# Optimization experiments

Measured on AMD Instinct MI355X. Metric: run time of the kernel, lower is better.

Reference implementation:

```python
import jax, jax.numpy as jnp
import numpy as np

WINDOWS = [2, 4, 6]
THR = 0.5


def conv1x1(x, w, b):
    # x: [N,C,H,W], w: [O,C], b: [O]
    return jnp.einsum('nchw,oc->nohw', x, w) + b[None, :, None, None]


def cpool(x):
    # channel max + mean -> [N,2,H,W]
    return jnp.stack([x.max(axis=1), x.mean(axis=1)], axis=1)


def mask_fusion(orin, feature, w1, b1, w2, b2):
    sim = jax.nn.sigmoid(jnp.sum(conv1x1(cpool(orin), w1, b1) * conv1x1(cpool(feature), w2, b2), axis=1, keepdims=True))
    mask = (sim > THR).astype(orin.dtype)
    return mask * feature + (1.0 - mask) * orin


def unfold(x, kh, kw, sh, sw, w):
    # torch F.unfold equivalent -> [N, C*kh*kw, w*w] (channel-major like torch)
    rows = jnp.arange(w)[:, None] * sh + jnp.arange(kh)[None, :]  # [w,kh]
    cols = jnp.arange(w)[:, None] * sw + jnp.arange(kw)[None, :]  # [w,kw]
    p = x[:, :, rows[:, :, None, None], cols[None, None, :, :]]  # [N,C,w,kh,w,kw]
    p = p.transpose(0, 1, 3, 5, 2, 4)  # [N,C,kh,kw,w,w]
    N, C = x.shape[:2]
    return p.reshape(N, C * kh * kw, w * w)


def fold(cols_, H, W, kh, kw, sh, sw, w):
    # torch F.fold equivalent (col2im with overlap-add)
    N, CK, P = cols_.shape
    C = CK // (kh * kw)
    p = cols_.reshape(N, C, kh, kw, w, w).transpose(0, 1, 4, 2, 5, 3).reshape(N, C, w * kh, w * kw)
    r = (jnp.arange(w)[:, None] * sh + jnp.arange(kh)[None, :]).reshape(-1)
    c = (jnp.arange(w)[:, None] * sw + jnp.arange(kw)[None, :]).reshape(-1)
    return jnp.zeros((N, C, H, W), cols_.dtype).at[:, :, r[:, None], c[None, :]].add(p)


def psa(u, wq, wk, wv):
    # u: [N,C,P,L]; scaled dot-product self-attention over L within each patch
    t = u.transpose(0, 2, 3, 1)  # [N,P,L,C]
    q, k, v = t @ wq, t @ wk, t @ wv
    s = jnp.einsum('nplc,npmc->nplm', q, k) / jnp.sqrt(jnp.asarray(t.shape[-1], t.dtype))
    o = jnp.einsum('nplm,npmc->nplc', jax.nn.softmax(s, axis=-1), v)
    return o.transpose(0, 3, 1, 2)


def setup_inputs():
    key = jax.random.key(0)
    ks = jax.random.split(key, 20)
    N, C, H, W = 4, 64, 72, 72
    E = len(WINDOWS) * C
    nrm = lambda k, shape, s: jax.random.normal(k, shape, jnp.float32) * s
    return {
        'x': nrm(ks[0], (N, C, H, W), 1.0),
        'exp_w': nrm(ks[1], (E, C), C ** -0.5), 'exp_b': jnp.zeros((E,), jnp.float32),
        'res_w': nrm(ks[2], (C, E), E ** -0.5), 'res_b': jnp.zeros((C,), jnp.float32),
        'fus_w': nrm(ks[3], (C, C), C ** -0.5), 'fus_b': jnp.zeros((C,), jnp.float32),
        'wq': nrm(ks[4], (C, C), C ** -0.5),
        'wk': nrm(ks[5], (C, C), C ** -0.5),
        'wv': nrm(ks[6], (C, C), C ** -0.5),
        'mf1a_w': nrm(ks[7], (2, 2), 0.7), 'mf1a_b': jnp.zeros((2,), jnp.float32),
        'mf1b_w': nrm(ks[8], (2, 2), 0.7), 'mf1b_b': jnp.zeros((2,), jnp.float32),
        'mf2a_w': nrm(ks[9], (2, 2), 0.7), 'mf2a_b': jnp.zeros((2,), jnp.float32),
        'mf2b_w': nrm(ks[10], (2, 2), 0.7), 'mf2b_b': jnp.zeros((2,), jnp.float32),
    }


def reference(x, exp_w, exp_b, res_w, res_b, fus_w, fus_b, wq, wk, wv,
              mf1a_w, mf1a_b, mf1b_w, mf1b_b, mf2a_w, mf2a_b, mf2b_w, mf2b_b):
    N, C, H, W = x.shape
    expx = conv1x1(x, exp_w, exp_b)  # [N, 3C, H, W]
    parts = jnp.split(expx, len(WINDOWS), axis=1)
    outs = []
    for i, w in enumerate(WINDOWS):
        sh, sw = H // w, W // w
        kh, kw = sh + H % w, sw + W % w
        u = unfold(parts[i], kh, kw, sh, sw, w)       # [N, C*kh*kw, w*w]
        u = u.reshape(N, C, w * w, kh * kw)           # raw reinterpret, as in torch .view
        a = psa(u, wq, wk, wv).reshape(N, C * kh * kw, w * w)
        cnt = fold(jnp.ones_like(a), H, W, kh, kw, sh, sw, w)
        outs.append(fold(a, H, W, kh, kw, sh, sw, w) / cnt)
    out = mask_fusion(jnp.concatenate(outs, axis=1), expx, mf1a_w, mf1a_b, mf1b_w, mf1b_b)
    out = conv1x1(out, res_w, res_b)
    out = mask_fusion(out, x, mf2a_w, mf2a_b, mf2b_w, mf2b_b)
    return conv1x1(out, fus_w, fus_b)
```

## Files before the change

kernel.cpp:

```cpp
#include <hip/hip_runtime.h>

constexpr int CN = 4;
constexpr int CC = 64;
constexpr int CH = 72, CW = 72;
constexpr int HW = CH * CW;
constexpr int NPOS = CN * HW;
constexpr long TOKF = 3L * NPOS * 64;
constexpr long HPAD = 4096;

typedef _Float16 h4 __attribute__((ext_vector_type(4)));
typedef _Float16 h8 __attribute__((ext_vector_type(8)));
typedef float f4 __attribute__((ext_vector_type(4)));

__device__ __forceinline__ int fidx(int row, int g, int off) {
  return (row << 6) + ((g ^ (row & 7)) << 3) + off;
}
__device__ __forceinline__ int f192(int row, int g) {
  return row * 192 + (((g & 24) | ((g ^ row) & 7)) << 3);
}

template <int WW, int SS>
__device__ __forceinline__ void expand_body(const float* __restrict__ x,
                                            const float* __restrict__ w64,
                                            const float* __restrict__ b64,
                                            float* __restrict__ out, int pg,
                                            int og0) {
  int n = pg / HW;
  int pos = pg - n * HW;
  int h = pos / CW, wcol = pos % CW;

  float xv[64];
  const float* xp = x + (long)n * CC * HW + pos;
#pragma unroll
  for (int c = 0; c < 64; ++c) xv[c] = xp[c * HW];

  int wr = h / SS, kx = h % SS, wcq = wcol / SS, ky = wcol % SS;
  int j = kx * (SS * WW * WW) + ky * (WW * WW) + wr * WW + wcq;
  float* op = out + ((long)n * HW + j) * 64;

#pragma unroll
  for (int og = og0; og < og0 + 4; ++og) {
    float t0[4];
#pragma unroll
    for (int i = 0; i < 4; ++i) {
      int o = og * 4 + i;
      float acc = b64[o];
      const float* wp = w64 + o * 64;
#pragma unroll
      for (int cg = 0; cg < 16; ++cg) {
        float4 w4 = *(const float4*)(wp + 4 * cg);
        acc = fmaf(xv[4 * cg + 0], w4.x, acc);
        acc = fmaf(xv[4 * cg + 1], w4.y, acc);
        acc = fmaf(xv[4 * cg + 2], w4.z, acc);
        acc = fmaf(xv[4 * cg + 3], w4.w, acc);
      }
      t0[i] = acc;
    }
    *(float4*)(op + og * 4) = make_float4(t0[0], t0[1], t0[2], t0[3]);
  }
}

__global__ __launch_bounds__(256) void k_prep(
    const float* __restrict__ x, const float* __restrict__ exp_w,
    const float* __restrict__ exp_b, const float* __restrict__ wq,
    const float* __restrict__ wk, const float* __restrict__ wv,
    const float* __restrict__ res_w, const float* __restrict__ fus_w,
    float* __restrict__ ex, _Float16* __restrict__ wTh,
    _Float16* __restrict__ wTl, _Float16* __restrict__ rwh,
    _Float16* __restrict__ rwl, _Float16* __restrict__ fwh,
    _Float16* __restrict__ fwl) {
  int b = blockIdx.x;
  if (b >= 972) {
    int i = (b - 972) * 256 + threadIdx.x;
    float v;
    _Float16 *dh, *dl;
    int off;
    if (i < 12288) {
      int m = i >> 12;
      int r = i & 4095;
      int cp = r >> 6, c = r & 63;
      const float* src = (m == 0) ? wq : ((m == 1) ? wk : wv);
      v = src[c * 64 + cp];
      dh = wTh; dl = wTl; off = i;
    } else if (i < 24576) {
      off = i - 12288;
      v = res_w[off];
      dh = rwh; dl = rwl;
    } else {
      off = i - 24576;
      v = fus_w[off];
      dh = fwh; dl = fwl;
    }
    _Float16 h = (_Float16)v;
    dh[off] = h;
    dl[off] = (_Float16)(v - (float)h);
    return;
  }
  int wi = b / 324;
  int b2 = b - wi * 324;
  int og0 = (b2 / 81) * 4;
  int pg = (b2 % 81) * 256 + threadIdx.x;
  if (wi == 0)
    expand_body<2, 36>(x, exp_w, exp_b, ex, pg, og0);
  else if (wi == 1)
    expand_body<4, 18>(x, exp_w + 4096, exp_b + 64, ex + (long)NPOS * 64, pg,
                       og0);
  else
    expand_body<6, 12>(x, exp_w + 8192, exp_b + 128, ex + 2L * NPOS * 64, pg,
                       og0);
}

__global__ __launch_bounds__(256) void k_qkv(
    const float* __restrict__ ex, const _Float16* __restrict__ wTh,
    const _Float16* __restrict__ wTl, _Float16* __restrict__ qh,
    _Float16* __restrict__ ql, _Float16* __restrict__ kh,
    _Float16* __restrict__ kl, _Float16* __restrict__ vth,
    _Float16* __restrict__ vtl) {
  __shared__ __align__(16) _Float16 Wh[12288], Wl[12288];
  __shared__ __align__(16) float Cb[4096];
  _Float16* Eh = (_Float16*)Cb;
  _Float16* El = (_Float16*)Cb + 4096;

  const int tid = threadIdx.x;
  const long tok0 = (long)blockIdx.x * 64;
  const int lane = tid & 63, w = tid >> 6;
  const int lw = lane & 15, lg = lane >> 4;

  {
    int srow = tid >> 2, sfq = tid & 3;
#pragma unroll
    for (int p = 0; p < 4; ++p) {
      int c0 = (4 * p + sfq) * 4;
      float4 v = *(const float4*)(ex + (tok0 + srow) * 64 + c0);
      h4 hh = {(_Float16)v.x, (_Float16)v.y, (_Float16)v.z, (_Float16)v.w};
      h4 ll = {(_Float16)(v.x - (float)hh[0]), (_Float16)(v.y - (float)hh[1]),
               (_Float16)(v.z - (float)hh[2]), (_Float16)(v.w - (float)hh[3])};
      *(h4*)&Eh[fidx(srow, c0 >> 3, c0 & 7)] = hh;
      *(h4*)&El[fidx(srow, c0 >> 3, c0 & 7)] = ll;
    }
  }
#pragma unroll
  for (int it = 0; it < 6; ++it) {
    int idx = it * 256 + tid;
    int row = idx >> 3, gr = idx & 7;
    *(h8*)&Wh[fidx(row, gr, 0)] = *(const h8*)(wTh + idx * 8);
    *(h8*)&Wl[fidx(row, gr, 0)] = *(const h8*)(wTl + idx * 8);
  }
  __syncthreads();

  h8 eh[2], el[2];
#pragma unroll
  for (int s = 0; s < 2; ++s) {
    eh[s] = *(const h8*)&Eh[fidx(w * 16 + lw, s * 4 + lg, 0)];
    el[s] = *(const h8*)&El[fidx(w * 16 + lw, s * 4 + lg, 0)];
  }
  __syncthreads();

  const float SC = 0.125f * 1.4426950408889634f;
#pragma unroll 1
  for (int p = 0; p < 3; ++p) {
#pragma unroll
    for (int ot = 0; ot < 4; ++ot) {
      f4 acc = (f4){0.f, 0.f, 0.f, 0.f};
#pragma unroll
      for (int s = 0; s < 2; ++s) {
        h8 bh = *(const h8*)&Wh[fidx(p * 64 + ot * 16 + lw, s * 4 + lg, 0)];
        h8 bl = *(const h8*)&Wl[fidx(p * 64 + ot * 16 + lw, s * 4 + lg, 0)];
        acc = __builtin_amdgcn_mfma_f32_16x16x32_f16(eh[s], bh, acc, 0, 0, 0);
        acc = __builtin_amdgcn_mfma_f32_16x16x32_f16(el[s], bh, acc, 0, 0, 0);
        acc = __builtin_amdgcn_mfma_f32_16x16x32_f16(eh[s], bl, acc, 0, 0, 0);
      }
#pragma unroll
      for (int r = 0; r < 4; ++r) {
        int row = w * 16 + 4 * lg + r;
        int col = ot * 16 + lw;
        Cb[(row << 6) + ((((col >> 2) ^ (row & 15))) << 2) + (col & 3)] =
            acc[r];
      }
    }
    __syncthreads();

    if (p < 2) {
      int tokl = tid >> 2, off = (tid & 3) * 16;
      float vals[16];
#pragma unroll
      for (int j = 0; j < 4; ++j) {
        int slot = (off >> 2) + j;
        f4 v = *(const f4*)&Cb[(tokl << 6) + (((slot ^ (tokl & 15))) << 2)];
        vals[4 * j + 0] = v[0]; vals[4 * j + 1] = v[1];
        vals[4 * j + 2] = v[2]; vals[4 * j + 3] = v[3];
      }
      float sc = (p == 0) ? SC : 1.0f;
      _Float16* dh = (p == 0 ? qh : kh) + (tok0 + tokl) * 64 + off;
      _Float16* dl = (p == 0 ? ql : kl) + (tok0 + tokl) * 64 + off;
      h8 hh0, hh1, ll0, ll1;
#pragma unroll
      for (int j = 0; j < 8; ++j) {
        float x0 = vals[j] * sc;
        _Float16 h = (_Float16)x0;
        hh0[j] = h;
        ll0[j] = (_Float16)(x0 - (float)h);
        float x1 = vals[8 + j] * sc;
        _Float16 h1 = (_Float16)x1;
        hh1[j] = h1;
        ll1[j] = (_Float16)(x1 - (float)h1);
      }
      *(h8*)dh = hh0; *(h8*)(dh + 8) = hh1;
      *(h8*)dl = ll0; *(h8*)(dl + 8) = ll1;
    } else {
      int ch0 = (tid & 15) * 4, tokl0 = (tid >> 4) * 4;
      float tv[4][4];
#pragma unroll
      for (int r = 0; r < 4; ++r) {
        int row = tokl0 + r;
        int slot = (ch0 >> 2) ^ (row & 15);
        f4 v = *(const f4*)&Cb[(row << 6) + (slot << 2)];
        tv[r][0] = v[0]; tv[r][1] = v[1]; tv[r][2] = v[2]; tv[r][3] = v[3];
      }
      long tokg = tok0 + tokl0;
      int wi = (int)(tokg / NPOS);
      long tl = tokg - (long)wi * NPOS;
      int L = (wi == 0) ? 1296 : ((wi == 1) ? 324 : 144);
      int g = (int)(tl / L);
      int key0 = (int)(tl - (long)g * L);
      long base = (long)wi * NPOS * 64 + (long)g * 64 * L + key0;
#pragma unroll
      for (int i = 0; i < 4; ++i) {
        h4 hh, ll;
#pragma unroll
        for (int r = 0; r < 4; ++r) {
          _Float16 h = (_Float16)tv[r][i];
          hh[r] = h;
          ll[r] = (_Float16)(tv[r][i] - (float)h);
        }
        *(h4*)&vth[base + (long)(ch0 + i) * L] = hh;
        *(h4*)&vtl[base + (long)(ch0 + i) * L] = ll;
      }
    }
    __syncthreads();
  }
}

__global__ __launch_bounds__(256) void k_attn(
    const _Float16* __restrict__ qg, const _Float16* __restrict__ qgl,
    const _Float16* __restrict__ kg, const _Float16* __restrict__ kgl,
    const _Float16* __restrict__ vg, const _Float16* __restrict__ vgl,
    float* __restrict__ og_) {
  __shared__ __align__(16) _Float16 Kh[4096], Kl[4096];
  __shared__ __align__(16) _Float16 Vh[4096], Vl[4096];
  __shared__ __align__(16) _Float16 Ph[4096], Pl[4096];

  const int tid = threadIdx.x;
  int b = blockIdx.x;
  int L, g, qt, NCH;
  long tokbase, vbase;
  if (b < 336) {
    L = 1296; NCH = 21; g = b & 15; qt = b >> 4;
    tokbase = (long)g * 1296;
    vbase = (long)g * 1296 * 64;
  } else if (b < 720) {
    int t = b - 336;
    L = 324; NCH = 6; g = t & 63; qt = t >> 6;
    tokbase = (long)NPOS + (long)g * 324;
    vbase = (long)NPOS * 64 + (long)g * 324 * 64;
  } else {
    int t = b - 720;
    L = 144; NCH = 3; g = t % 144; qt = t / 144;
    tokbase = 2L * NPOS + (long)g * 144;
    vbase = 2L * NPOS * 64 + (long)g * 144 * 64;
  }

  const int lane = tid & 63, w = tid >> 6;
  const int lw = lane & 15, lg = lane >> 4;
  const int w16 = w * 16;

  h8 qfh[2], qfl[2];
  {
    long qb = (tokbase + (long)qt * 64 + w16 + lw) * 64;
#pragma unroll
    for (int s = 0; s < 2; ++s) {
      qfh[s] = *(const h8*)(qg + qb + (s * 4 + lg) * 8);
      qfl[s] = *(const h8*)(qgl + qb + (s * 4 + lg) * 8);
    }
  }

  float m_s = -1e30f, l_s = 0.f;
  f4 oa[4];
#pragma unroll
  for (int i = 0; i < 4; ++i) oa[i] = (f4){0.f, 0.f, 0.f, 0.f};

  const int krow = tid >> 3, kgr = tid & 7;
  const long ksA = (tokbase + krow) * 64 + kgr * 8;
  const long vsA = vbase + (long)krow * L + kgr * 8;
  const long v32 = (long)32 * L;

  h8 rk0, rk1, rl0, rl1, rv0, rv1, rw0, rw1;
  auto loadKV = [&](int chn) {
    long ko = ksA + ((long)chn << 12);
    long vo = vsA + chn * 64;
    rk0 = *(const h8*)(kg + ko);
    rl0 = *(const h8*)(kgl + ko);
    rv0 = *(const h8*)(vg + vo);
    rw0 = *(const h8*)(vgl + vo);
    rk1 = *(const h8*)(kg + ko + 2048);
    rl1 = *(const h8*)(kgl + ko + 2048);
    rv1 = *(const h8*)(vg + vo + v32);
    rw1 = *(const h8*)(vgl + vo + v32);
  };
  loadKV(0);

  for (int ch = 0; ch < NCH; ++ch) {
    __syncthreads();
    {
      *(h8*)&Kh[fidx(krow, kgr, 0)] = rk0;
      *(h8*)&Kl[fidx(krow, kgr, 0)] = rl0;
      *(h8*)&Vh[fidx(krow, kgr, 0)] = rv0;
      *(h8*)&Vl[fidx(krow, kgr, 0)] = rw0;
      *(h8*)&Kh[fidx(32 + krow, kgr, 0)] = rk1;
      *(h8*)&Kl[fidx(32 + krow, kgr, 0)] = rl1;
      *(h8*)&Vh[fidx(32 + krow, kgr, 0)] = rv1;
      *(h8*)&Vl[fidx(32 + krow, kgr, 0)] = rw1;
    }
    __syncthreads();
    if (ch + 1 < NCH) loadKV(ch + 1);

    f4 sa[4];
#pragma unroll
    for (int kt = 0; kt < 4; ++kt) sa[kt] = (f4){0.f, 0.f, 0.f, 0.f};
#pragma unroll
    for (int slab = 0; slab < 2; ++slab) {
      h8 qbh = qfh[slab];
      h8 qbl = qfl[slab];
#pragma unroll
      for (int kt = 0; kt < 4; ++kt) {
        h8 ah = *(const h8*)&Kh[fidx(kt * 16 + lw, slab * 4 + lg, 0)];
        h8 al = *(const h8*)&Kl[fidx(kt * 16 + lw, slab * 4 + lg, 0)];
        sa[kt] = __builtin_amdgcn_mfma_f32_16x16x32_f16(ah, qbh, sa[kt], 0, 0, 0);
        sa[kt] = __builtin_amdgcn_mfma_f32_16x16x32_f16(al, qbh, sa[kt], 0, 0, 0);
        sa[kt] = __builtin_amdgcn_mfma_f32_16x16x32_f16(ah, qbl, sa[kt], 0, 0, 0);
      }
    }

    float pr[4][4];
    float pmax = -1e30f;
#pragma unroll
    for (int kt = 0; kt < 4; ++kt)
#pragma unroll
      for (int r = 0; r < 4; ++r) {
        int kidx = ch * 64 + kt * 16 + 4 * lg + r;
        float s = (kidx < L) ? sa[kt][r] : -1e30f;
        pr[kt][r] = s;
        pmax = fmaxf(pmax, s);
      }
    pmax = fmaxf(pmax, __shfl_xor(pmax, 16));
    pmax = fmaxf(pmax, __shfl_xor(pmax, 32));
    if (!__all(pmax <= m_s + 8.0f)) {
      float mn = fmaxf(m_s, pmax);
      float fs = exp2f(m_s - mn);
      m_s = mn;
      float fsb[4];
#pragma unroll
      for (int r = 0; r < 4; ++r) fsb[r] = __shfl(fs, 4 * lg + r);
#pragma unroll
      for (int ct = 0; ct < 4; ++ct)
#pragma unroll
        for (int r = 0; r < 4; ++r) oa[ct][r] *= fsb[r];
      l_s *= fs;
    }
    float rs = 0.f;
#pragma unroll
    for (int kt = 0; kt < 4; ++kt)
#pragma unroll
      for (int r = 0; r < 4; ++r) {
        float e = exp2f(pr[kt][r] - m_s);
        pr[kt][r] = e;
        rs += e;
      }
    rs += __shfl_xor(rs, 16);
    rs += __shfl_xor(rs, 32);
    l_s += rs;

#pragma unroll
    for (int kt = 0; kt < 4; ++kt) {
      h4 hh = {(_Float16)pr[kt][0], (_Float16)pr[kt][1], (_Float16)pr[kt][2],
               (_Float16)pr[kt][3]};
      h4 ll = {(_Float16)(pr[kt][0] - (float)hh[0]),
               (_Float16)(pr[kt][1] - (float)hh[1]),
               (_Float16)(pr[kt][2] - (float)hh[2]),
               (_Float16)(pr[kt][3] - (float)hh[3])};
      int key0 = kt * 16 + 4 * lg;
      int kgr2 = key0 >> 3, ko = key0 & 7;
      *(h4*)&Ph[fidx(w16 + lw, kgr2, ko)] = hh;
      *(h4*)&Pl[fidx(w16 + lw, kgr2, ko)] = ll;
    }

#pragma unroll
    for (int slab = 0; slab < 2; ++slab) {
      h8 pah = *(const h8*)&Ph[fidx(w16 + lw, slab * 4 + lg, 0)];
      h8 pal = *(const h8*)&Pl[fidx(w16 + lw, slab * 4 + lg, 0)];
#pragma unroll
      for (int ct = 0; ct < 4; ++ct) {
        h8 vbh = *(const h8*)&Vh[fidx(ct * 16 + lw, slab * 4 + lg, 0)];
        h8 vbl = *(const h8*)&Vl[fidx(ct * 16 + lw, slab * 4 + lg, 0)];
        oa[ct] = __builtin_amdgcn_mfma_f32_16x16x32_f16(pah, vbh, oa[ct], 0, 0, 0);
        oa[ct] = __builtin_amdgcn_mfma_f32_16x16x32_f16(pal, vbh, oa[ct], 0, 0, 0);
        oa[ct] = __builtin_amdgcn_mfma_f32_16x16x32_f16(pah, vbl, oa[ct], 0, 0, 0);
      }
    }
  }

  float linv[4];
#pragma unroll
  for (int r = 0; r < 4; ++r) linv[r] = 1.0f / __shfl(l_s, 4 * lg + r);
#pragma unroll
  for (int r = 0; r < 4; ++r) {
    int qi = qt * 64 + w16 + 4 * lg + r;
    if (qi < L) {
      float* op = og_ + (tokbase + qi) * 64 + lw;
#pragma unroll
      for (int ct = 0; ct < 4; ++ct) op[ct * 16] = oa[ct][r] * linv[r];
    }
  }
}

__global__ __launch_bounds__(256) void k_fuse3(
    const float* __restrict__ x, const float* __restrict__ ex,
    const float* __restrict__ att, const float* __restrict__ m1aw,
    const float* __restrict__ m1ab, const float* __restrict__ m1bw,
    const float* __restrict__ m1bb, const _Float16* __restrict__ rwh,
    const _Float16* __restrict__ rwl, const float* __restrict__ res_b,
    const _Float16* __restrict__ fwh, const _Float16* __restrict__ fwl,
    const float* __restrict__ fus_b, const float* __restrict__ m2aw,
    const float* __restrict__ m2ab, const float* __restrict__ m2bw,
    const float* __restrict__ m2bb, float* __restrict__ out) {
  __shared__ __align__(16) _Float16 F1hS[12288];
  __shared__ __align__(16) _Float16 F1lS[12288];
  float* Cb = (float*)F1hS;
  _Float16* o2h = F1lS;
  _Float16* o2l = F1lS + 4096;

  const int tid = threadIdx.x;
  const int posb = blockIdx.x * 64;
  const int n = posb / HW, posn = posb % HW;
  const int lane = tid & 63, w = tid >> 6;
  const int lw = lane & 15, lg = lane >> 4;
  const int w16 = w * 16;

  {
    float w1a0 = m1aw[0], w1a1 = m1aw[1], w1a2 = m1aw[2], w1a3 = m1aw[3];
    float b1a0 = m1ab[0], b1a1 = m1ab[1];
    float w1b0 = m1bw[0], w1b1 = m1bw[1], w1b2 = m1bw[2], w1b3 = m1bw[3];
    float b1b0 = m1bb[0], b1b1 = m1bb[1];
#pragma unroll 2
    for (int pp = 0; pp < 16; ++pp) {
      int pl = w * 16 + pp;
      int pos = posn + pl;
      int h = pos / CW, wcol = pos % CW;
      auto tok = [&](int S, int W) -> int {
        int wr = h / S, kx = h % S, wcq = wcol / S, ky = wcol % S;
        return kx * (S * W * W) + ky * (W * W) + wr * W + wcq;
      };
      int j0 = tok(36, 2), j1 = tok(18, 4), j2 = tok(12, 6);
      long t0 = ((long)n * HW + j0) * 64 + lane;
      long t1 = ((long)NPOS + (long)n * HW + j1) * 64 + lane;
      long t2 = (2L * NPOS + (long)n * HW + j2) * 64 + lane;
      float av0 = att[t0], av1 = att[t1], av2 = att[t2];
      float ev0 = ex[t0], ev1 = ex[t1], ev2 = ex[t2];
      float mxa = fmaxf(fmaxf(av0, av1), av2), sma = av0 + av1 + av2;
      float mxe = fmaxf(fmaxf(ev0, ev1), ev2), sme = ev0 + ev1 + ev2;
#pragma unroll
      for (int d = 1; d < 64; d <<= 1) {
        mxa = fmaxf(mxa, __shfl_xor(mxa, d));
        sma += __shfl_xor(sma, d);
        mxe = fmaxf(mxe, __shfl_xor(mxe, d));
        sme += __shfl_xor(sme, d);
      }
      float mna = sma * (1.f / 192.f), mne = sme * (1.f / 192.f);
      float ca0 = fmaf(w1a0, mxa, fmaf(w1a1, mna, b1a0));
      float ca1 = fmaf(w1a2, mxa, fmaf(w1a3, mna, b1a1));
      float cb0 = fmaf(w1b0, mxe, fmaf(w1b1, mne, b1b0));
      float cb1 = fmaf(w1b2, mxe, fmaf(w1b3, mne, b1b1));
      bool mk = (ca0 * cb0 + ca1 * cb1) > 0.f;
      float v0 = mk ? ev0 : av0;
      float v1 = mk ? ev1 : av1;
      float v2 = mk ? ev2 : av2;
      _Float16 h0 = (_Float16)v0, h1 = (_Float16)v1, h2 = (_Float16)v2;
      int c0 = lane, c1 = lane + 64, c2 = lane + 128;
      F1hS[f192(pl, c0 >> 3) + (c0 & 7)] = h0;
      F1lS[f192(pl, c0 >> 3) + (c0 & 7)] = (_Float16)(v0 - (float)h0);
      F1hS[f192(pl, c1 >> 3) + (c1 & 7)] = h1;
      F1lS[f192(pl, c1 >> 3) + (c1 & 7)] = (_Float16)(v1 - (float)h1);
      F1hS[f192(pl, c2 >> 3) + (c2 & 7)] = h2;
      F1lS[f192(pl, c2 >> 3) + (c2 & 7)] = (_Float16)(v2 - (float)h2);
    }
  }
  __syncthreads();

  h8 ah[6], al[6];
#pragma unroll
  for (int s = 0; s < 6; ++s) {
    ah[s] = *(const h8*)&F1hS[f192(w16 + lw, s * 4 + lg)];
    al[s] = *(const h8*)&F1lS[f192(w16 + lw, s * 4 + lg)];
  }

  f4 acc[4];
#pragma unroll
  for (int ot = 0; ot < 4; ++ot) {
    float bb = res_b[ot * 16 + lw];
    acc[ot] = (f4){bb, bb, bb, bb};
#pragma unroll
    for (int s = 0; s < 6; ++s) {
      int wo = (ot * 16 + lw) * 192 + (s * 4 + lg) * 8;
      h8 bh = *(const h8*)(rwh + wo);
      h8 bl = *(const h8*)(rwl + wo);
      acc[ot] = __builtin_amdgcn_mfma_f32_16x16x32_f16(ah[s], bh, acc[ot], 0, 0, 0);
      acc[ot] = __builtin_amdgcn_mfma_f32_16x16x32_f16(al[s], bh, acc[ot], 0, 0, 0);
      acc[ot] = __builtin_amdgcn_mfma_f32_16x16x32_f16(ah[s], bl, acc[ot], 0, 0, 0);
    }
  }
  __syncthreads();

#pragma unroll
  for (int ot = 0; ot < 4; ++ot)
#pragma unroll
    for (int r = 0; r < 4; ++r) {
      int row = w16 + 4 * lg + r, col = ot * 16 + lw;
      Cb[(row << 6) + ((((col >> 2) ^ (row & 15))) << 2) + (col & 3)] =
          acc[ot][r];
    }
  __syncthreads();

  const int pos = tid >> 2, off = (tid & 3) * 16;
  float vals[16];
#pragma unroll
  for (int j = 0; j < 4; ++j) {
    int slot = (off >> 2) + j;
    f4 v = *(const f4*)&Cb[(pos << 6) + (((slot ^ (pos & 15))) << 2)];
    vals[4 * j + 0] = v[0]; vals[4 * j + 1] = v[1];
    vals[4 * j + 2] = v[2]; vals[4 * j + 3] = v[3];
  }
  float amx = vals[0], asum = vals[0];
#pragma unroll
  for (int i = 1; i < 16; ++i) {
    amx = fmaxf(amx, vals[i]);
    asum += vals[i];
  }
  amx = fmaxf(amx, __shfl_xor(amx, 1)); asum += __shfl_xor(asum, 1);
  amx = fmaxf(amx, __shfl_xor(amx, 2)); asum += __shfl_xor(asum, 2);
  float xv[16];
  const float* xp = x + ((long)n * CC + off) * HW + posn + pos;
#pragma unroll
  for (int i = 0; i < 16; ++i) xv[i] = xp[i * HW];
  float xmx = xv[0], xsum = xv[0];
#pragma unroll
  for (int i = 1; i < 16; ++i) {
    xmx = fmaxf(xmx, xv[i]);
    xsum += xv[i];
  }
  xmx = fmaxf(xmx, __shfl_xor(xmx, 1)); xsum += __shfl_xor(xsum, 1);
  xmx = fmaxf(xmx, __shfl_xor(xmx, 2)); xsum += __shfl_xor(xsum, 2);
  float rmn = asum * (1.f / 64.f), xmn = xsum * (1.f / 64.f);
  float ca0 = fmaf(m2aw[0], amx, fmaf(m2aw[1], rmn, m2ab[0]));
  float ca1 = fmaf(m2aw[2], amx, fmaf(m2aw[3], rmn, m2ab[1]));
  float cb0 = fmaf(m2bw[0], xmx, fmaf(m2bw[1], xmn, m2bb[0]));
  float cb1 = fmaf(m2bw[2], xmx, fmaf(m2bw[3], xmn, m2bb[1]));
  bool mk2 = (ca0 * cb0 + ca1 * cb1) > 0.f;

#pragma unroll
  for (int hf = 0; hf < 2; ++hf) {
    h8 hh, ll;
#pragma unroll
    for (int j = 0; j < 8; ++j) {
      float v = mk2 ? xv[hf * 8 + j] : vals[hf * 8 + j];
      _Float16 hx = (_Float16)v;
      hh[j] = hx;
      ll[j] = (_Float16)(v - (float)hx);
    }
    int g = (off >> 3) + hf;
    *(h8*)&o2h[fidx(pos, g, 0)] = hh;
    *(h8*)&o2l[fidx(pos, g, 0)] = ll;
  }
  __syncthreads();

  h8 a2h[2], a2l[2];
#pragma unroll
  for (int s = 0; s < 2; ++s) {
    a2h[s] = *(const h8*)&o2h[fidx(w16 + lw, s * 4 + lg, 0)];
    a2l[s] = *(const h8*)&o2l[fidx(w16 + lw, s * 4 + lg, 0)];
  }
  f4 acc2[4];
#pragma unroll
  for (int ot = 0; ot < 4; ++ot) {
    float bb = fus_b[ot * 16 + lw];
    acc2[ot] = (f4){bb, bb, bb, bb};
#pragma unroll
    for (int s = 0; s < 2; ++s) {
      int wo = (ot * 16 + lw) * 64 + (s * 4 + lg) * 8;
      h8 bh = *(const h8*)(fwh + wo);
      h8 bl = *(const h8*)(fwl + wo);
      acc2[ot] = __builtin_amdgcn_mfma_f32_16x16x32_f16(a2h[s], bh, acc2[ot], 0, 0, 0);
      acc2[ot] = __builtin_amdgcn_mfma_f32_16x16x32_f16(a2l[s], bh, acc2[ot], 0, 0, 0);
      acc2[ot] = __builtin_amdgcn_mfma_f32_16x16x32_f16(a2h[s], bl, acc2[ot], 0, 0, 0);
    }
  }
  __syncthreads();

#pragma unroll
  for (int ot = 0; ot < 4; ++ot)
#pragma unroll
    for (int r = 0; r < 4; ++r) {
      int prow = w16 + 4 * lg + r, col = ot * 16 + lw;
      Cb[(prow << 6) + ((col + prow) & 63)] = acc2[ot][r];
    }
  __syncthreads();
#pragma unroll
  for (int i = 0; i < 16; ++i) {
    float v = Cb[(lane << 6) + ((w16 + i + lane) & 63)];
    out[((long)n * CC + w16 + i) * HW + posn + lane] = v;
  }
}

extern "C" void kernel_launch(void* const* d_in, const int* in_sizes, int n_in,
                              void* d_out, int out_size, void* d_ws,
                              size_t ws_size, hipStream_t stream) {
  (void)in_sizes; (void)n_in; (void)out_size;
  const float* x      = (const float*)d_in[0];
  const float* exp_w  = (const float*)d_in[1];
  const float* exp_b  = (const float*)d_in[2];
  const float* res_w  = (const float*)d_in[3];
  const float* res_b  = (const float*)d_in[4];
  const float* fus_w  = (const float*)d_in[5];
  const float* fus_b  = (const float*)d_in[6];
  const float* wq     = (const float*)d_in[7];
  const float* wk     = (const float*)d_in[8];
  const float* wv     = (const float*)d_in[9];
  const float* m1aw   = (const float*)d_in[10];
  const float* m1ab   = (const float*)d_in[11];
  const float* m1bw   = (const float*)d_in[12];
  const float* m1bb   = (const float*)d_in[13];
  const float* m2aw   = (const float*)d_in[14];
  const float* m2ab   = (const float*)d_in[15];
  const float* m2bw   = (const float*)d_in[16];
  const float* m2bb   = (const float*)d_in[17];

  const long HSZ = TOKF + HPAD;
  const size_t needF =
      2 * (size_t)TOKF + (6 * (size_t)HSZ + 2 * 12288 + 2 * 12288 + 2 * 4096) / 2;
  if (ws_size < needF * sizeof(float)) return;
  float* ws = (float*)d_ws;
  float* ex = ws;
  float* ob = ex + TOKF;
  _Float16* qh  = (_Float16*)(ob + TOKF);
  _Float16* ql  = qh + HSZ;
  _Float16* kh  = ql + HSZ;
  _Float16* kl  = kh + HSZ;
  _Float16* vth = kl + HSZ;
  _Float16* vtl = vth + HSZ;
  _Float16* wTh = vtl + HSZ;
  _Float16* wTl = wTh + 12288;
  _Float16* rwh = wTl + 12288;
  _Float16* rwl = rwh + 12288;
  _Float16* fwh = rwl + 12288;
  _Float16* fwl = fwh + 4096;

  k_prep<<<1084, 256, 0, stream>>>(x, exp_w, exp_b, wq, wk, wv, res_w, fus_w,
                                   ex, wTh, wTl, rwh, rwl, fwh, fwl);
  k_qkv<<<972, 256, 0, stream>>>(ex, wTh, wTl, qh, ql, kh, kl, vth, vtl);
  k_attn<<<1152, 256, 0, stream>>>(qh, ql, kh, kl, vth, vtl, ob);
  k_fuse3<<<324, 256, 0, stream>>>(x, ex, ob, m1aw, m1ab, m1bw, m1bb, rwh,
                                   rwl, res_b, fwh, fwl, fus_b, m2aw, m2ab,
                                   m2bw, m2bb, (float*)d_out);
}
```

Baseline: 139.6 us.

## Load attention K/V MFMA fragments directly from global memory instead of LDS

The attention kernel no longer stages K and V tiles through shared memory with register prefetch and two barriers per chunk. Each wave now reads its MFMA operand fragments for K and V straight from global memory, relying on L1/L2 caching for reuse across the four waves in a block. This removes the LDS writes, the barriers and 32KB of LDS, which may raise occupancy. In exchange every wave issues its own global loads, with no software prefetch to hide their latency.

```diff
diff --git a/kernel.cpp b/kernel.cpp
--- a/kernel.cpp
+++ b/kernel.cpp
@@ -246,8 +246,6 @@
     const _Float16* __restrict__ kg, const _Float16* __restrict__ kgl,
     const _Float16* __restrict__ vg, const _Float16* __restrict__ vgl,
     float* __restrict__ og_) {
-  __shared__ __align__(16) _Float16 Kh[4096], Kl[4096];
-  __shared__ __align__(16) _Float16 Vh[4096], Vl[4096];
   __shared__ __align__(16) _Float16 Ph[4096], Pl[4096];
 
   const int tid = threadIdx.x;
@@ -289,40 +287,13 @@
 #pragma unroll
   for (int i = 0; i < 4; ++i) oa[i] = (f4){0.f, 0.f, 0.f, 0.f};
 
-  const int krow = tid >> 3, kgr = tid & 7;
-  const long ksA = (tokbase + krow) * 64 + kgr * 8;
-  const long vsA = vbase + (long)krow * L + kgr * 8;
-  const long v32 = (long)32 * L;
-
-  h8 rk0, rk1, rl0, rl1, rv0, rv1, rw0, rw1;
-  auto loadKV = [&](int chn) {
-    long ko = ksA + ((long)chn << 12);
-    long vo = vsA + chn * 64;
-    rk0 = *(const h8*)(kg + ko);
-    rl0 = *(const h8*)(kgl + ko);
-    rv0 = *(const h8*)(vg + vo);
-    rw0 = *(const h8*)(vgl + vo);
-    rk1 = *(const h8*)(kg + ko + 2048);
-    rl1 = *(const h8*)(kgl + ko + 2048);
-    rv1 = *(const h8*)(vg + vo + v32);
-    rw1 = *(const h8*)(vgl + vo + v32);
-  };
-  loadKV(0);
+  const long kfb = (tokbase + lw) * 64 + lg * 8;
+  const long vfb = vbase + (long)lw * L + lg * 8;
+  const long vctL = (long)16 * L;
 
   for (int ch = 0; ch < NCH; ++ch) {
-    __syncthreads();
-    {
-      *(h8*)&Kh[fidx(krow, kgr, 0)] = rk0;
-      *(h8*)&Kl[fidx(krow, kgr, 0)] = rl0;
-      *(h8*)&Vh[fidx(krow, kgr, 0)] = rv0;
-      *(h8*)&Vl[fidx(krow, kgr, 0)] = rw0;
-      *(h8*)&Kh[fidx(32 + krow, kgr, 0)] = rk1;
-      *(h8*)&Kl[fidx(32 + krow, kgr, 0)] = rl1;
-      *(h8*)&Vh[fidx(32 + krow, kgr, 0)] = rv1;
-      *(h8*)&Vl[fidx(32 + krow, kgr, 0)] = rw1;
-    }
-    __syncthreads();
-    if (ch + 1 < NCH) loadKV(ch + 1);
+    const long kc = kfb + ((long)ch << 12);
+    const long vc = vfb + ch * 64;
 
     f4 sa[4];
 #pragma unroll
@@ -333,8 +304,9 @@
       h8 qbl = qfl[slab];
 #pragma unroll
       for (int kt = 0; kt < 4; ++kt) {
-        h8 ah = *(const h8*)&Kh[fidx(kt * 16 + lw, slab * 4 + lg, 0)];
-        h8 al = *(const h8*)&Kl[fidx(kt * 16 + lw, slab * 4 + lg, 0)];
+        long ka = kc + kt * 1024 + slab * 32;
+        h8 ah = *(const h8*)(kg + ka);
+        h8 al = *(const h8*)(kgl + ka);
         sa[kt] = __builtin_amdgcn_mfma_f32_16x16x32_f16(ah, qbh, sa[kt], 0, 0, 0);
         sa[kt] = __builtin_amdgcn_mfma_f32_16x16x32_f16(al, qbh, sa[kt], 0, 0, 0);
         sa[kt] = __builtin_amdgcn_mfma_f32_16x16x32_f16(ah, qbl, sa[kt], 0, 0, 0);
@@ -400,8 +372,9 @@
       h8 pal = *(const h8*)&Pl[fidx(w16 + lw, slab * 4 + lg, 0)];
 #pragma unroll
       for (int ct = 0; ct < 4; ++ct) {
-        h8 vbh = *(const h8*)&Vh[fidx(ct * 16 + lw, slab * 4 + lg, 0)];
-        h8 vbl = *(const h8*)&Vl[fidx(ct * 16 + lw, slab * 4 + lg, 0)];
+        long va = vc + ct * vctL + slab * 32;
+        h8 vbh = *(const h8*)(vg + va);
+        h8 vbl = *(const h8*)(vgl + va);
         oa[ct] = __builtin_amdgcn_mfma_f32_16x16x32_f16(pah, vbh, oa[ct], 0, 0, 0);
         oa[ct] = __builtin_amdgcn_mfma_f32_16x16x32_f16(pal, vbh, oa[ct], 0, 0, 0);
         oa[ct] = __builtin_amdgcn_mfma_f32_16x16x32_f16(pah, vbl, oa[ct], 0, 0, 0);
```

Measured after the change: 228.6 us. 63.7% more time.
